# Performance work log

Measured on AMD Instinct MI355X. Metric: run time of the kernel, lower is better.

The kernel has to match this reference:

```python
import jax, jax.numpy as jnp
import numpy as np

FACTOR = 5


def setup_inputs() -> dict:
    key = jax.random.key(0)
    k1, k2, k3, k4 = jax.random.split(key, 4)
    B, L, H, D = 2, 4096, 8, 64
    sample_k = min(FACTOR * int(np.ceil(np.log(L))), L)  # 45
    return {
        "queries": jax.random.normal(k1, (B, L, H, D), dtype=jnp.float32),
        "keys": jax.random.normal(k2, (B, L, H, D), dtype=jnp.float32),
        "values": jax.random.normal(k3, (B, L, H, D), dtype=jnp.float32),
        "attn_mask": jnp.zeros((1,), dtype=bool),  # unused; ProbMask is built internally
        "index_sample": jax.random.randint(k4, (L, sample_k), 0, L, dtype=jnp.int32),
    }


def reference(queries, keys, values, attn_mask, index_sample):
    # queries/keys/values: [B, L, H, D] -> [B, H, L, D]
    Q = jnp.swapaxes(queries, 1, 2)
    K = jnp.swapaxes(keys, 1, 2)
    V = jnp.swapaxes(values, 1, 2)
    B, H, L_Q, D = Q.shape
    L_K = K.shape[2]
    n_top = min(FACTOR * int(np.ceil(np.log(L_Q))), L_Q)
    scale = 1.0 / jnp.sqrt(jnp.float32(D))

    # --- sparse measurement: sampled QK scores ---
    # K_sample[b,h,q,s,d] = K[b,h,index_sample[q,s],d]
    K_sample = K[:, :, index_sample, :]                       # [B,H,L_Q,S,D]
    QK_sample = jnp.einsum("bhqd,bhqsd->bhqs", Q, K_sample)   # [B,H,L_Q,S]
    M = QK_sample.max(axis=-1) - QK_sample.sum(axis=-1) / L_K  # sparsity measure

    # --- top-u query selection ---
    _, M_top = jax.lax.top_k(M, n_top)                         # [B,H,u]
    Q_reduce = jnp.take_along_axis(Q, M_top[..., None], axis=2)  # [B,H,u,D]

    # --- full scores for selected queries ---
    scores = jnp.einsum("bhud,bhkd->bhuk", Q_reduce, K) * scale  # [B,H,u,L_K]

    # mask_flag=True: causal ProbMask (key pos > selected query pos)
    key_pos = jnp.arange(L_K)
    causal = key_pos[None, None, None, :] > M_top[..., None]
    scores = jnp.where(causal, -jnp.inf, scores)
    attn = jax.nn.softmax(scores, axis=-1)

    # --- initial context (cumsum, masked case) + scatter update ---
    context = jnp.cumsum(V, axis=2)                            # [B,H,L_Q,D]
    ctx_sel = jnp.einsum("bhuk,bhkd->bhud", attn, V)
    b_idx = jnp.arange(B)[:, None, None]
    h_idx = jnp.arange(H)[None, :, None]
    context = context.at[b_idx, h_idx, M_top].set(ctx_sel)
    return jnp.swapaxes(context, 1, 2)  # [B, L_Q, H, D]
```

## Files before the change

kernel.cpp:

```cpp
#include <hip/hip_runtime.h>
#include <math.h>

#define B_    2
#define L_    4096
#define H_    8
#define D_    64
#define S_    45
#define NT_   45
#define BH_   16
#define CHV   64
#define NCHV  64
#define KC    128
#define NKC   32
#define SCALE 0.125f
#define NEG_BIG (-1e30f)

#define OFF_M     0
#define OFF_MTOP  65536
#define OFF_MPART 66304
#define OFF_SPART 89344
#define OFF_CTXP  112384
#define OFF_VSUM  112384

template <int CTRL>
__device__ __forceinline__ float dpp_ror_f(float x) {
    int y = __builtin_amdgcn_update_dpp(0, __float_as_int(x), CTRL, 0xF, 0xF, false);
    return __int_as_float(y);
}

__device__ __forceinline__ unsigned short f2bf(float x) {
    return (unsigned short)(__float_as_uint(x) >> 16);
}
__device__ __forceinline__ float bflo(unsigned u) { return __uint_as_float(u << 16); }
__device__ __forceinline__ float bfhi(unsigned u) { return __uint_as_float(u & 0xffff0000u); }

__global__ __launch_bounds__(256) void k1(const float* __restrict__ Q,
                                          const float* __restrict__ Kt,
                                          const float* __restrict__ V,
                                          const int* __restrict__ samp,
                                          float* __restrict__ ws)
{
    int tid  = threadIdx.x;
    int w    = tid >> 6;
    int lane = tid & 63;

    if (blockIdx.x < 4096) {
        int i   = blockIdx.x;
        int xcd = i & 7;
        int b   = xcd >> 2;
        int hh  = (xcd >> 1) & 1;
        int qq  = ((i >> 3) << 1) | (xcd & 1);

        __shared__ int soff[4][S_];
        if (tid < 4 * S_) {
            int qs = tid / S_, ss = tid - qs * S_;
            soff[qs][ss] = samp[(qq * 4 + qs) * S_ + ss] << 11;
        }
        __syncthreads();

        int q  = qq * 4 + w;
        int h4 = lane >> 4;

        const float4 q4 = *(const float4*)(Q +
            ((((long)b * L_ + q) * H_ + hh * 4) << 6) + lane * 4);

        const char* kb_base = (const char*)Kt +
            (long)b * L_ * 2048 + hh * 1024 + lane * 16;

        float mx = NEG_BIG, sm = 0.f;
#pragma unroll
        for (int jb = 0; jb < 45; jb += 15) {
            float4 kb[15];
#pragma unroll
            for (int j = 0; j < 15; ++j)
                kb[j] = *(const float4*)(kb_base + soff[w][jb + j]);
#pragma unroll
            for (int j = 0; j < 15; ++j) {
                float p = q4.x * kb[j].x + q4.y * kb[j].y +
                          q4.z * kb[j].z + q4.w * kb[j].w;
                p += dpp_ror_f<0x121>(p);
                p += dpp_ror_f<0x122>(p);
                p += dpp_ror_f<0x124>(p);
                p += dpp_ror_f<0x128>(p);
                mx = fmaxf(mx, p);
                sm += p;
            }
        }
        if ((lane & 15) == 0)
            ws[OFF_M + ((long)(b * 8 + hh * 4 + h4)) * L_ + q] =
                mx - sm * (1.0f / (float)L_);
    } else {
        int unit = (blockIdx.x - 4096) * 4 + w;
        int bh = unit >> 6, ch = unit & 63;
        int b = bh >> 3, h = bh & 7;
        const float* vp = V + ((((long)b * L_ + (long)ch * CHV) * H_ + h) << 6) + lane;
        float ssum = 0.f;
#pragma unroll
        for (int ib = 0; ib < CHV; ib += 16) {
            float vb[16];
#pragma unroll
            for (int j = 0; j < 16; ++j) vb[j] = vp[(long)(ib + j) * (H_ * D_)];
#pragma unroll
            for (int j = 0; j < 16; ++j) ssum += vb[j];
        }
        ws[OFF_VSUM + unit * 64 + lane] = ssum;
    }
}

__global__ __launch_bounds__(256) void k2(const float* __restrict__ V,
                                          float* __restrict__ out,
                                          float* __restrict__ ws)
{
    int tid  = threadIdx.x;
    int w    = tid >> 6;
    int lane = tid & 63;

    if (blockIdx.x < 16) {
        int bh = blockIdx.x;
        int* Mtop = (int*)ws + OFF_MTOP + bh * NT_;

        __shared__ float lv_[4][NT_];
        __shared__ int   li_[4][NT_];

        const float4* m4 = (const float4*)(ws + OFF_M + (long)bh * L_ +
                                           w * 1024 + lane * 16);
        float vals[16];
        {
            float4 a = m4[0], bq = m4[1], c = m4[2], d = m4[3];
            vals[0]=a.x; vals[1]=a.y; vals[2]=a.z; vals[3]=a.w;
            vals[4]=bq.x; vals[5]=bq.y; vals[6]=bq.z; vals[7]=bq.w;
            vals[8]=c.x; vals[9]=c.y; vals[10]=c.z; vals[11]=c.w;
            vals[12]=d.x; vals[13]=d.y; vals[14]=d.z; vals[15]=d.w;
        }
        float lv = NEG_BIG; int li = lane * 16;
#pragma unroll
        for (int j = 0; j < 16; ++j)
            if (vals[j] > lv) { lv = vals[j]; li = lane * 16 + j; }

        for (int r = 0; r < NT_; ++r) {
            float rm = lv;
            rm = fmaxf(rm, dpp_ror_f<0x121>(rm));
            rm = fmaxf(rm, dpp_ror_f<0x122>(rm));
            rm = fmaxf(rm, dpp_ror_f<0x124>(rm));
            rm = fmaxf(rm, dpp_ror_f<0x128>(rm));
            rm = fmaxf(rm, __shfl_xor(rm, 16));
            rm = fmaxf(rm, __shfl_xor(rm, 32));
            unsigned long long bm = __ballot(lv == rm);
            int winner = __ffsll(bm) - 1;
            int wi = __shfl(li, winner);
            if (lane == 0) { lv_[w][r] = rm; li_[w][r] = w * 1024 + wi; }
            if (lane == winner) {
#pragma unroll
                for (int j = 0; j < 16; ++j)
                    if (j == (wi & 15)) vals[j] = NEG_BIG;
                lv = NEG_BIG; li = lane * 16;
#pragma unroll
                for (int j = 0; j < 16; ++j)
                    if (vals[j] > lv) { lv = vals[j]; li = lane * 16 + j; }
            }
        }
        __syncthreads();

        if (w == 0) {
            int g = lane & 3;
            int p = 0;
            float hv = lv_[g][0]; int hi = li_[g][0];
            for (int r = 0; r < NT_; ++r) {
                float v0 = __shfl(hv, 0), v1 = __shfl(hv, 1),
                      v2 = __shfl(hv, 2), v3 = __shfl(hv, 3);
                int   i0 = __shfl(hi, 0), i1 = __shfl(hi, 1),
                      i2 = __shfl(hi, 2), i3 = __shfl(hi, 3);
                float bv = v0; int bi = i0, bg = 0;
                if (v1 > bv) { bv = v1; bi = i1; bg = 1; }
                if (v2 > bv) { bv = v2; bi = i2; bg = 2; }
                if (v3 > bv) { bv = v3; bi = i3; bg = 3; }
                if (lane == 0) Mtop[r] = bi;
                if (g == bg) {
                    ++p;
                    hv = (p < NT_) ? lv_[g][p] : NEG_BIG;
                    hi = (p < NT_) ? li_[g][p] : 0;
                }
            }
        }
    } else {
        int unit = (blockIdx.x - 16) * 4 + w;
        int bh = unit >> 6, ch = unit & 63;
        int b = bh >> 3, h = bh & 7;
        int d = lane;

        float acc = 0.f;
        {
            const float* vs = ws + OFF_VSUM + (long)bh * NCHV * 64 + d;
            int c = 0;
            for (; c + 8 <= ch; c += 8) {
                float vb[8];
#pragma unroll
                for (int j = 0; j < 8; ++j) vb[j] = vs[(c + j) * 64];
#pragma unroll
                for (int j = 0; j < 8; ++j) acc += vb[j];
            }
            for (; c < ch; ++c) acc += vs[c * 64];
        }

        const float* vp = V   + ((((long)b * L_ + (long)ch * CHV) * H_ + h) << 6) + d;
        float*       op = out + ((((long)b * L_ + (long)ch * CHV) * H_ + h) << 6) + d;
#pragma unroll
        for (int ib = 0; ib < CHV; ib += 16) {
            float vb[16];
#pragma unroll
            for (int j = 0; j < 16; ++j) vb[j] = vp[(long)(ib + j) * (H_ * D_)];
#pragma unroll
            for (int j = 0; j < 16; ++j) {
                acc += vb[j];
                op[(long)(ib + j) * (H_ * D_)] = acc;
            }
        }
    }
}

#define KPAD16 72
#define NUH    23
__global__ __launch_bounds__(256) void kC(const float* __restrict__ Q,
                                          const float* __restrict__ Kt,
                                          const float* __restrict__ V,
                                          float* __restrict__ ws)
{
    __shared__ unsigned short Klds16[KC * KPAD16];
    __shared__ unsigned short P16[NUH * KC];
    __shared__ int qpos[NUH];

    int tid = threadIdx.x;
    int bh = blockIdx.x >> 6;
    int kc = (blockIdx.x >> 1) & 31;
    int ug = blockIdx.x & 1;
    int b = bh >> 3, h = bh & 7;
    int kbase = kc * KC;
    int u0 = ug * 23;
    int NU = ug ? 22 : 23;

    if (tid < NU) qpos[tid] = ((const int*)ws)[OFF_MTOP + bh * NT_ + tid + u0];

    {
        const float4* ksrc4 = (const float4*)(Kt + ((((long)b * L_ + kbase) * H_ + h) << 6));
#pragma unroll
        for (int i = 0; i < 8; ++i) {
            int e = i * 256 + tid;
            int r = e >> 4, c4 = e & 15;
            float4 kv = ksrc4[(long)r * (H_ * D_ / 4) + c4];
            uint2 pk;
            pk.x = (__float_as_uint(kv.x) >> 16) | (__float_as_uint(kv.y) & 0xffff0000u);
            pk.y = (__float_as_uint(kv.z) >> 16) | (__float_as_uint(kv.w) & 0xffff0000u);
            *(uint2*)&Klds16[r * KPAD16 + c4 * 4] = pk;
        }
    }
    __syncthreads();

    int k = tid & 127, uh = tid >> 7;
    int kpos = kbase + k;
    {
        float kf[64];
#pragma unroll
        for (int j = 0; j < 8; ++j) {
            uint4 U = *(const uint4*)&Klds16[k * KPAD16 + j * 8];
            kf[j*8+0] = bflo(U.x); kf[j*8+1] = bfhi(U.x);
            kf[j*8+2] = bflo(U.y); kf[j*8+3] = bfhi(U.y);
            kf[j*8+4] = bflo(U.z); kf[j*8+5] = bfhi(U.z);
            kf[j*8+6] = bflo(U.w); kf[j*8+7] = bfhi(U.w);
        }

#pragma unroll 3
        for (int j = 0; j < 12; ++j) {
            int ul = uh * 12 + j;
            if (ul > NU - 1) ul = NU - 1;
            int qp_ = __builtin_amdgcn_readfirstlane(qpos[ul]);
            const float4* qrow = (const float4*)(Q + ((((long)b * L_ + qp_) * H_ + h) << 6));
            float a0 = 0.f, a1 = 0.f, a2 = 0.f, a3 = 0.f;
#pragma unroll
            for (int jj = 0; jj < 16; jj += 4) {
                float4 q0 = qrow[jj + 0], q1 = qrow[jj + 1];
                float4 q2 = qrow[jj + 2], q3 = qrow[jj + 3];
                a0 += q0.x * kf[jj*4+ 0] + q0.y * kf[jj*4+ 1] +
                      q0.z * kf[jj*4+ 2] + q0.w * kf[jj*4+ 3];
                a1 += q1.x * kf[jj*4+ 4] + q1.y * kf[jj*4+ 5] +
                      q1.z * kf[jj*4+ 6] + q1.w * kf[jj*4+ 7];
                a2 += q2.x * kf[jj*4+ 8] + q2.y * kf[jj*4+ 9] +
                      q2.z * kf[jj*4+10] + q2.w * kf[jj*4+11];
                a3 += q3.x * kf[jj*4+12] + q3.y * kf[jj*4+13] +
                      q3.z * kf[jj*4+14] + q3.w * kf[jj*4+15];
            }
            float sc = ((a0 + a1) + (a2 + a3)) * SCALE;
            if (kpos > qp_) sc = NEG_BIG;
            P16[ul * KC + k] = f2bf(sc);
        }
    }
    __syncthreads();

    int lane = tid & 63, w = tid >> 6;
    for (int ul = w; ul < NU; ul += 4) {
        float s0 = bflo(P16[ul * KC + lane]);
        float s1 = bflo(P16[ul * KC + 64 + lane]);
        float m = fmaxf(s0, s1);
#pragma unroll
        for (int off = 32; off; off >>= 1) m = fmaxf(m, __shfl_xor(m, off));
        float e0 = __expf(s0 - m), e1 = __expf(s1 - m);
        unsigned short b0 = f2bf(e0), b1 = f2bf(e1);
        P16[ul * KC + lane]      = b0;
        P16[ul * KC + 64 + lane] = b1;
        float sm = bflo(b0) + bflo(b1);
#pragma unroll
        for (int off = 32; off; off >>= 1) sm += __shfl_xor(sm, off);
        if (lane == 0) {
            ws[OFF_MPART + ((long)bh * NT_ + u0 + ul) * NKC + kc] = m;
            ws[OFF_SPART + ((long)bh * NT_ + u0 + ul) * NKC + kc] = sm;
        }
    }
    __syncthreads();

    {
        const float* vsrc = V + ((((long)b * L_ + kbase) * H_ + h) << 6);
        float ctx[6];
#pragma unroll
        for (int j = 0; j < 6; ++j) ctx[j] = 0.f;
        for (int kk8 = 0; kk8 < 16; ++kk8) {
            float v[8];
#pragma unroll
            for (int t = 0; t < 8; ++t)
                v[t] = vsrc[(long)(kk8 * 8 + t) * (H_ * D_) + lane];
#pragma unroll
            for (int j = 0; j < 6; ++j) {
                int ul = w + j * 4;
                if (ul < NU) {
                    uint4 U = *(const uint4*)&P16[ul * KC + kk8 * 8];
                    ctx[j] += bflo(U.x) * v[0] + bfhi(U.x) * v[1]
                            + bflo(U.y) * v[2] + bfhi(U.y) * v[3]
                            + bflo(U.z) * v[4] + bfhi(U.z) * v[5]
                            + bflo(U.w) * v[6] + bfhi(U.w) * v[7];
                }
            }
        }
#pragma unroll
        for (int j = 0; j < 6; ++j) {
            int ul = w + j * 4;
            if (ul < NU)
                ws[OFF_CTXP + ((long)(bh * NKC + kc) * NT_ + u0 + ul) * 64 + lane] = ctx[j];
        }
    }
}

__global__ __launch_bounds__(64) void kD(float* __restrict__ out,
                                         const float* __restrict__ ws)
{
    int lane = threadIdx.x;
    int unit = blockIdx.x;
    int bh = unit / NT_, u = unit - bh * NT_;
    int b = bh >> 3, h = bh & 7;

    const float4* mp4 = (const float4*)(ws + OFF_MPART + ((long)bh * NT_ + u) * NKC);
    const float4* sp4 = (const float4*)(ws + OFF_SPART + ((long)bh * NT_ + u) * NKC);

    float mc[NKC], sc[NKC];
    float m = NEG_BIG;
#pragma unroll
    for (int c4 = 0; c4 < NKC / 4; ++c4) {
        float4 mv = mp4[c4];
        float4 sv = sp4[c4];
        mc[c4 * 4 + 0] = mv.x; mc[c4 * 4 + 1] = mv.y;
        mc[c4 * 4 + 2] = mv.z; mc[c4 * 4 + 3] = mv.w;
        sc[c4 * 4 + 0] = sv.x; sc[c4 * 4 + 1] = sv.y;
        sc[c4 * 4 + 2] = sv.z; sc[c4 * 4 + 3] = sv.w;
        m = fmaxf(m, fmaxf(fmaxf(mv.x, mv.y), fmaxf(mv.z, mv.w)));
    }
    float T = 0.f, ctx = 0.f;
#pragma unroll
    for (int c = 0; c < NKC; ++c) {
        float wgt = __expf(mc[c] - m);
        T   += sc[c] * wgt;
        ctx += ws[OFF_CTXP + ((long)(bh * NKC + c) * NT_ + u) * 64 + lane] * wgt;
    }
    int qp = ((const int*)ws)[OFF_MTOP + bh * NT_ + u];
    out[((((long)b * L_ + qp) * H_ + h) << 6) + lane] = ctx / T;
}

extern "C" void kernel_launch(void* const* d_in, const int* in_sizes, int n_in,
                              void* d_out, int out_size, void* d_ws, size_t ws_size,
                              hipStream_t stream)
{
    const float* Q    = (const float*)d_in[0];
    const float* K    = (const float*)d_in[1];
    const float* V    = (const float*)d_in[2];
    const int*   samp = (const int*)d_in[4];
    float* out = (float*)d_out;
    float* ws  = (float*)d_ws;

    k1<<<4352, 256, 0, stream>>>(Q, K, V, samp, ws);
    k2<<<272, 256, 0, stream>>>(V, out, ws);
    kC<<<1024, 256, 0, stream>>>(Q, K, V, ws);
    kD<<<720, 64, 0, stream>>>(out, ws);
}
```

Baseline: 188.9 us.

## Process two queries per wave in sampling kernel and move cumsum into attention kernel

The sampled-score kernel now has each wave handle two queries, which halves its block count and gives each wave more independent gather loads in flight. The cumsum-output work moves out of the top-k kernel and into the attention kernel as extra blocks, so the top-k kernel runs only its 16 blocks and the cumsum overlaps with the attention blocks. The context-partial workspace offset is moved so it no longer aliases the V-sum region, which the cumsum blocks now read while attention blocks write partials. The cost is more register pressure per wave in the sampling kernel and extra shared-memory footprint reserved for the cumsum blocks in the attention kernel.

Result: slower. 196.5 us (+4.0%).

```diff
diff --git a/kernel.cpp b/kernel.cpp
--- a/kernel.cpp
+++ b/kernel.cpp
@@ -19,8 +19,8 @@
 #define OFF_MTOP  65536
 #define OFF_MPART 66304
 #define OFF_SPART 89344
-#define OFF_CTXP  112384
 #define OFF_VSUM  112384
+#define OFF_CTXP  177920
 
 template <int CTRL>
 __device__ __forceinline__ float dpp_ror_f(float x) {
@@ -44,53 +44,71 @@
     int w    = tid >> 6;
     int lane = tid & 63;
 
-    if (blockIdx.x < 4096) {
+    if (blockIdx.x < 2048) {
         int i   = blockIdx.x;
         int xcd = i & 7;
         int b   = xcd >> 2;
         int hh  = (xcd >> 1) & 1;
-        int qq  = ((i >> 3) << 1) | (xcd & 1);
-
-        __shared__ int soff[4][S_];
-        if (tid < 4 * S_) {
-            int qs = tid / S_, ss = tid - qs * S_;
-            soff[qs][ss] = samp[(qq * 4 + qs) * S_ + ss] << 11;
-        }
+        int qg  = ((i >> 3) << 1) | (xcd & 1);
+
+        __shared__ int soff[8 * S_];
+        for (int e = tid; e < 8 * S_; e += 256)
+            soff[e] = samp[qg * (8 * S_) + e] << 11;
         __syncthreads();
 
-        int q  = qq * 4 + w;
+        int qa = qg * 8 + w * 2;
         int h4 = lane >> 4;
 
-        const float4 q4 = *(const float4*)(Q +
-            ((((long)b * L_ + q) * H_ + hh * 4) << 6) + lane * 4);
+        const float4 qva = *(const float4*)(Q +
+            ((((long)b * L_ + qa)     * H_ + hh * 4) << 6) + lane * 4);
+        const float4 qvb = *(const float4*)(Q +
+            ((((long)b * L_ + qa + 1) * H_ + hh * 4) << 6) + lane * 4);
 
         const char* kb_base = (const char*)Kt +
             (long)b * L_ * 2048 + hh * 1024 + lane * 16;
-
-        float mx = NEG_BIG, sm = 0.f;
-#pragma unroll
-        for (int jb = 0; jb < 45; jb += 15) {
-            float4 kb[15];
-#pragma unroll
-            for (int j = 0; j < 15; ++j)
-                kb[j] = *(const float4*)(kb_base + soff[w][jb + j]);
-#pragma unroll
-            for (int j = 0; j < 15; ++j) {
-                float p = q4.x * kb[j].x + q4.y * kb[j].y +
-                          q4.z * kb[j].z + q4.w * kb[j].w;
+        const int* sa = &soff[(w * 2) * S_];
+        const int* sb = sa + S_;
+
+        float mxa = NEG_BIG, sma = 0.f, mxb = NEG_BIG, smb = 0.f;
+#pragma unroll
+        for (int jb = 0; jb < 45; jb += 9) {
+            float4 ka[9], kb[9];
+#pragma unroll
+            for (int j = 0; j < 9; ++j)
+                ka[j] = *(const float4*)(kb_base + sa[jb + j]);
+#pragma unroll
+            for (int j = 0; j < 9; ++j)
+                kb[j] = *(const float4*)(kb_base + sb[jb + j]);
+#pragma unroll
+            for (int j = 0; j < 9; ++j) {
+                float p = qva.x * ka[j].x + qva.y * ka[j].y +
+                          qva.z * ka[j].z + qva.w * ka[j].w;
                 p += dpp_ror_f<0x121>(p);
                 p += dpp_ror_f<0x122>(p);
                 p += dpp_ror_f<0x124>(p);
                 p += dpp_ror_f<0x128>(p);
-                mx = fmaxf(mx, p);
-                sm += p;
-            }
-        }
-        if ((lane & 15) == 0)
-            ws[OFF_M + ((long)(b * 8 + hh * 4 + h4)) * L_ + q] =
-                mx - sm * (1.0f / (float)L_);
+                mxa = fmaxf(mxa, p);
+                sma += p;
+            }
+#pragma unroll
+            for (int j = 0; j < 9; ++j) {
+                float p = qvb.x * kb[j].x + qvb.y * kb[j].y +
+                          qvb.z * kb[j].z + qvb.w * kb[j].w;
+                p += dpp_ror_f<0x121>(p);
+                p += dpp_ror_f<0x122>(p);
+                p += dpp_ror_f<0x124>(p);
+                p += dpp_ror_f<0x128>(p);
+                mxb = fmaxf(mxb, p);
+                smb += p;
+            }
+        }
+        if ((lane & 15) == 0) {
+            long base = (long)(b * 8 + hh * 4 + h4) * L_;
+            ws[OFF_M + base + qa]     = mxa - sma * (1.0f / (float)L_);
+            ws[OFF_M + base + qa + 1] = mxb - smb * (1.0f / (float)L_);
+        }
     } else {
-        int unit = (blockIdx.x - 4096) * 4 + w;
+        int unit = (blockIdx.x - 2048) * 4 + w;
         int bh = unit >> 6, ch = unit & 63;
         int b = bh >> 3, h = bh & 7;
         const float* vp = V + ((((long)b * L_ + (long)ch * CHV) * H_ + h) << 6) + lane;
@@ -107,86 +125,99 @@
     }
 }
 
-__global__ __launch_bounds__(256) void k2(const float* __restrict__ V,
-                                          float* __restrict__ out,
-                                          float* __restrict__ ws)
+__global__ __launch_bounds__(256) void k2(float* __restrict__ ws)
 {
     int tid  = threadIdx.x;
     int w    = tid >> 6;
     int lane = tid & 63;
 
-    if (blockIdx.x < 16) {
-        int bh = blockIdx.x;
-        int* Mtop = (int*)ws + OFF_MTOP + bh * NT_;
-
-        __shared__ float lv_[4][NT_];
-        __shared__ int   li_[4][NT_];
-
-        const float4* m4 = (const float4*)(ws + OFF_M + (long)bh * L_ +
-                                           w * 1024 + lane * 16);
-        float vals[16];
-        {
-            float4 a = m4[0], bq = m4[1], c = m4[2], d = m4[3];
-            vals[0]=a.x; vals[1]=a.y; vals[2]=a.z; vals[3]=a.w;
-            vals[4]=bq.x; vals[5]=bq.y; vals[6]=bq.z; vals[7]=bq.w;
-            vals[8]=c.x; vals[9]=c.y; vals[10]=c.z; vals[11]=c.w;
-            vals[12]=d.x; vals[13]=d.y; vals[14]=d.z; vals[15]=d.w;
-        }
-        float lv = NEG_BIG; int li = lane * 16;
-#pragma unroll
-        for (int j = 0; j < 16; ++j)
-            if (vals[j] > lv) { lv = vals[j]; li = lane * 16 + j; }
-
+    int bh = blockIdx.x;
+    int* Mtop = (int*)ws + OFF_MTOP + bh * NT_;
+
+    __shared__ float lv_[4][NT_];
+    __shared__ int   li_[4][NT_];
+
+    const float4* m4 = (const float4*)(ws + OFF_M + (long)bh * L_ +
+                                       w * 1024 + lane * 16);
+    float vals[16];
+    {
+        float4 a = m4[0], bq = m4[1], c = m4[2], d = m4[3];
+        vals[0]=a.x; vals[1]=a.y; vals[2]=a.z; vals[3]=a.w;
+        vals[4]=bq.x; vals[5]=bq.y; vals[6]=bq.z; vals[7]=bq.w;
+        vals[8]=c.x; vals[9]=c.y; vals[10]=c.z; vals[11]=c.w;
+        vals[12]=d.x; vals[13]=d.y; vals[14]=d.z; vals[15]=d.w;
+    }
+    float lv = NEG_BIG; int li = lane * 16;
+#pragma unroll
+    for (int j = 0; j < 16; ++j)
+        if (vals[j] > lv) { lv = vals[j]; li = lane * 16 + j; }
+
+    for (int r = 0; r < NT_; ++r) {
+        float rm = lv;
+        rm = fmaxf(rm, dpp_ror_f<0x121>(rm));
+        rm = fmaxf(rm, dpp_ror_f<0x122>(rm));
+        rm = fmaxf(rm, dpp_ror_f<0x124>(rm));
+        rm = fmaxf(rm, dpp_ror_f<0x128>(rm));
+        rm = fmaxf(rm, __shfl_xor(rm, 16));
+        rm = fmaxf(rm, __shfl_xor(rm, 32));
+        unsigned long long bm = __ballot(lv == rm);
+        int winner = __ffsll(bm) - 1;
+        int wi = __shfl(li, winner);
+        if (lane == 0) { lv_[w][r] = rm; li_[w][r] = w * 1024 + wi; }
+        if (lane == winner) {
+#pragma unroll
+            for (int j = 0; j < 16; ++j)
+                if (j == (wi & 15)) vals[j] = NEG_BIG;
+            lv = NEG_BIG; li = lane * 16;
+#pragma unroll
+            for (int j = 0; j < 16; ++j)
+                if (vals[j] > lv) { lv = vals[j]; li = lane * 16 + j; }
+        }
+    }
+    __syncthreads();
+
+    if (w == 0) {
+        int g = lane & 3;
+        int p = 0;
+        float hv = lv_[g][0]; int hi = li_[g][0];
         for (int r = 0; r < NT_; ++r) {
-            float rm = lv;
-            rm = fmaxf(rm, dpp_ror_f<0x121>(rm));
-            rm = fmaxf(rm, dpp_ror_f<0x122>(rm));
-            rm = fmaxf(rm, dpp_ror_f<0x124>(rm));
-            rm = fmaxf(rm, dpp_ror_f<0x128>(rm));
-            rm = fmaxf(rm, __shfl_xor(rm, 16));
-            rm = fmaxf(rm, __shfl_xor(rm, 32));
-            unsigned long long bm = __ballot(lv == rm);
-            int winner = __ffsll(bm) - 1;
-            int wi = __shfl(li, winner);
-            if (lane == 0) { lv_[w][r] = rm; li_[w][r] = w * 1024 + wi; }
-            if (lane == winner) {
-#pragma unroll
-                for (int j = 0; j < 16; ++j)
-                    if (j == (wi & 15)) vals[j] = NEG_BIG;
-                lv = NEG_BIG; li = lane * 16;
-#pragma unroll
-                for (int j = 0; j < 16; ++j)
-                    if (vals[j] > lv) { lv = vals[j]; li = lane * 16 + j; }
-            }
-        }
-        __syncthreads();
-
-        if (w == 0) {
-            int g = lane & 3;
-            int p = 0;
-            float hv = lv_[g][0]; int hi = li_[g][0];
-            for (int r = 0; r < NT_; ++r) {
-                float v0 = __shfl(hv, 0), v1 = __shfl(hv, 1),
-                      v2 = __shfl(hv, 2), v3 = __shfl(hv, 3);
-                int   i0 = __shfl(hi, 0), i1 = __shfl(hi, 1),
-                      i2 = __shfl(hi, 2), i3 = __shfl(hi, 3);
-                float bv = v0; int bi = i0, bg = 0;
-                if (v1 > bv) { bv = v1; bi = i1; bg = 1; }
-                if (v2 > bv) { bv = v2; bi = i2; bg = 2; }
-                if (v3 > bv) { bv = v3; bi = i3; bg = 3; }
-                if (lane == 0) Mtop[r] = bi;
-                if (g == bg) {
-                    ++p;
-                    hv = (p < NT_) ? lv_[g][p] : NEG_BIG;
-                    hi = (p < NT_) ? li_[g][p] : 0;
-                }
-            }
-        }
-    } else {
-        int unit = (blockIdx.x - 16) * 4 + w;
+            float v0 = __shfl(hv, 0), v1 = __shfl(hv, 1),
+                  v2 = __shfl(hv, 2), v3 = __shfl(hv, 3);
+            int   i0 = __shfl(hi, 0), i1 = __shfl(hi, 1),
+                  i2 = __shfl(hi, 2), i3 = __shfl(hi, 3);
+            float bv = v0; int bi = i0, bg = 0;
+            if (v1 > bv) { bv = v1; bi = i1; bg = 1; }
+            if (v2 > bv) { bv = v2; bi = i2; bg = 2; }
+            if (v3 > bv) { bv = v3; bi = i3; bg = 3; }
+            if (lane == 0) Mtop[r] = bi;
+            if (g == bg) {
+                ++p;
+                hv = (p < NT_) ? lv_[g][p] : NEG_BIG;
+                hi = (p < NT_) ? li_[g][p] : 0;
+            }
+        }
+    }
+}
+
+#define KPAD16 72
+#define NUH    23
+__global__ __launch_bounds__(256) void k3(const float* __restrict__ Q,
+                                          const float* __restrict__ Kt,
+                                          const float* __restrict__ V,
+                                          float* __restrict__ out,
+                                          float* __restrict__ ws)
+{
+    __shared__ unsigned short Klds16[KC * KPAD16];
+    __shared__ unsigned short P16[NUH * KC];
+    __shared__ int qpos[NUH];
+
+    int tid = threadIdx.x;
+
+    if (blockIdx.x >= 1024) {
+        int w = tid >> 6, d = tid & 63;
+        int unit = (blockIdx.x - 1024) * 4 + w;
         int bh = unit >> 6, ch = unit & 63;
         int b = bh >> 3, h = bh & 7;
-        int d = lane;
 
         float acc = 0.f;
         {
@@ -215,21 +246,9 @@
                 op[(long)(ib + j) * (H_ * D_)] = acc;
             }
         }
-    }
-}
-
-#define KPAD16 72
-#define NUH    23
-__global__ __launch_bounds__(256) void kC(const float* __restrict__ Q,
-                                          const float* __restrict__ Kt,
-                                          const float* __restrict__ V,
-                                          float* __restrict__ ws)
-{
-    __shared__ unsigned short Klds16[KC * KPAD16];
-    __shared__ unsigned short P16[NUH * KC];
-    __shared__ int qpos[NUH];
-
-    int tid = threadIdx.x;
+        return;
+    }
+
     int bh = blockIdx.x >> 6;
     int kc = (blockIdx.x >> 1) & 31;
     int ug = blockIdx.x & 1;
@@ -392,8 +411,8 @@
     float* out = (float*)d_out;
     float* ws  = (float*)d_ws;
 
-    k1<<<4352, 256, 0, stream>>>(Q, K, V, samp, ws);
-    k2<<<272, 256, 0, stream>>>(V, out, ws);
-    kC<<<1024, 256, 0, stream>>>(Q, K, V, ws);
+    k1<<<2304, 256, 0, stream>>>(Q, K, V, samp, ws);
+    k2<<<16, 256, 0, stream>>>(ws);
+    k3<<<1280, 256, 0, stream>>>(Q, K, V, out, ws);
     kD<<<720, 64, 0, stream>>>(out, ws);
 }
```

## Skip fully causal-masked key chunks and overlap cumsum with attention kernel

Applied to the files above, without the earlier changes.

The prefix-sum output pass moves out of the top-k kernel and into extra blocks of the attention kernel. The top-k kernel now launches only its 16 selection blocks, and the cumsum writes can overlap the score and PV work. Inside the attention kernel, any selected query whose position lies before the key chunk skips its QK dot products and writes masked scores directly. Waves with no active queries skip the PV accumulation and the partial-context stores. The context-partials workspace gets its own offset so it no longer aliases the V chunk sums that are now read concurrently. The combining kernel still reads partial contexts for skipped chunks, which are left unwritten, so it relies on their zero weights to cancel them.

New measurement: 189.4 us. About the same (+0.3%).

```diff
diff --git a/kernel.cpp b/kernel.cpp
--- a/kernel.cpp
+++ b/kernel.cpp
@@ -19,8 +19,8 @@
 #define OFF_MTOP  65536
 #define OFF_MPART 66304
 #define OFF_SPART 89344
-#define OFF_CTXP  112384
 #define OFF_VSUM  112384
+#define OFF_CTXP  177920
 
 template <int CTRL>
 __device__ __forceinline__ float dpp_ror_f(float x) {
@@ -107,86 +107,99 @@
     }
 }
 
-__global__ __launch_bounds__(256) void k2(const float* __restrict__ V,
-                                          float* __restrict__ out,
-                                          float* __restrict__ ws)
+__global__ __launch_bounds__(256) void k2(float* __restrict__ ws)
 {
     int tid  = threadIdx.x;
     int w    = tid >> 6;
     int lane = tid & 63;
 
-    if (blockIdx.x < 16) {
-        int bh = blockIdx.x;
-        int* Mtop = (int*)ws + OFF_MTOP + bh * NT_;
-
-        __shared__ float lv_[4][NT_];
-        __shared__ int   li_[4][NT_];
-
-        const float4* m4 = (const float4*)(ws + OFF_M + (long)bh * L_ +
-                                           w * 1024 + lane * 16);
-        float vals[16];
-        {
-            float4 a = m4[0], bq = m4[1], c = m4[2], d = m4[3];
-            vals[0]=a.x; vals[1]=a.y; vals[2]=a.z; vals[3]=a.w;
-            vals[4]=bq.x; vals[5]=bq.y; vals[6]=bq.z; vals[7]=bq.w;
-            vals[8]=c.x; vals[9]=c.y; vals[10]=c.z; vals[11]=c.w;
-            vals[12]=d.x; vals[13]=d.y; vals[14]=d.z; vals[15]=d.w;
-        }
-        float lv = NEG_BIG; int li = lane * 16;
-#pragma unroll
-        for (int j = 0; j < 16; ++j)
-            if (vals[j] > lv) { lv = vals[j]; li = lane * 16 + j; }
-
+    int bh = blockIdx.x;
+    int* Mtop = (int*)ws + OFF_MTOP + bh * NT_;
+
+    __shared__ float lv_[4][NT_];
+    __shared__ int   li_[4][NT_];
+
+    const float4* m4 = (const float4*)(ws + OFF_M + (long)bh * L_ +
+                                       w * 1024 + lane * 16);
+    float vals[16];
+    {
+        float4 a = m4[0], bq = m4[1], c = m4[2], d = m4[3];
+        vals[0]=a.x; vals[1]=a.y; vals[2]=a.z; vals[3]=a.w;
+        vals[4]=bq.x; vals[5]=bq.y; vals[6]=bq.z; vals[7]=bq.w;
+        vals[8]=c.x; vals[9]=c.y; vals[10]=c.z; vals[11]=c.w;
+        vals[12]=d.x; vals[13]=d.y; vals[14]=d.z; vals[15]=d.w;
+    }
+    float lv = NEG_BIG; int li = lane * 16;
+#pragma unroll
+    for (int j = 0; j < 16; ++j)
+        if (vals[j] > lv) { lv = vals[j]; li = lane * 16 + j; }
+
+    for (int r = 0; r < NT_; ++r) {
+        float rm = lv;
+        rm = fmaxf(rm, dpp_ror_f<0x121>(rm));
+        rm = fmaxf(rm, dpp_ror_f<0x122>(rm));
+        rm = fmaxf(rm, dpp_ror_f<0x124>(rm));
+        rm = fmaxf(rm, dpp_ror_f<0x128>(rm));
+        rm = fmaxf(rm, __shfl_xor(rm, 16));
+        rm = fmaxf(rm, __shfl_xor(rm, 32));
+        unsigned long long bm = __ballot(lv == rm);
+        int winner = __ffsll(bm) - 1;
+        int wi = __shfl(li, winner);
+        if (lane == 0) { lv_[w][r] = rm; li_[w][r] = w * 1024 + wi; }
+        if (lane == winner) {
+#pragma unroll
+            for (int j = 0; j < 16; ++j)
+                if (j == (wi & 15)) vals[j] = NEG_BIG;
+            lv = NEG_BIG; li = lane * 16;
+#pragma unroll
+            for (int j = 0; j < 16; ++j)
+                if (vals[j] > lv) { lv = vals[j]; li = lane * 16 + j; }
+        }
+    }
+    __syncthreads();
+
+    if (w == 0) {
+        int g = lane & 3;
+        int p = 0;
+        float hv = lv_[g][0]; int hi = li_[g][0];
         for (int r = 0; r < NT_; ++r) {
-            float rm = lv;
-            rm = fmaxf(rm, dpp_ror_f<0x121>(rm));
-            rm = fmaxf(rm, dpp_ror_f<0x122>(rm));
-            rm = fmaxf(rm, dpp_ror_f<0x124>(rm));
-            rm = fmaxf(rm, dpp_ror_f<0x128>(rm));
-            rm = fmaxf(rm, __shfl_xor(rm, 16));
-            rm = fmaxf(rm, __shfl_xor(rm, 32));
-            unsigned long long bm = __ballot(lv == rm);
-            int winner = __ffsll(bm) - 1;
-            int wi = __shfl(li, winner);
-            if (lane == 0) { lv_[w][r] = rm; li_[w][r] = w * 1024 + wi; }
-            if (lane == winner) {
-#pragma unroll
-                for (int j = 0; j < 16; ++j)
-                    if (j == (wi & 15)) vals[j] = NEG_BIG;
-                lv = NEG_BIG; li = lane * 16;
-#pragma unroll
-                for (int j = 0; j < 16; ++j)
-                    if (vals[j] > lv) { lv = vals[j]; li = lane * 16 + j; }
-            }
-        }
-        __syncthreads();
-
-        if (w == 0) {
-            int g = lane & 3;
-            int p = 0;
-            float hv = lv_[g][0]; int hi = li_[g][0];
-            for (int r = 0; r < NT_; ++r) {
-                float v0 = __shfl(hv, 0), v1 = __shfl(hv, 1),
-                      v2 = __shfl(hv, 2), v3 = __shfl(hv, 3);
-                int   i0 = __shfl(hi, 0), i1 = __shfl(hi, 1),
-                      i2 = __shfl(hi, 2), i3 = __shfl(hi, 3);
-                float bv = v0; int bi = i0, bg = 0;
-                if (v1 > bv) { bv = v1; bi = i1; bg = 1; }
-                if (v2 > bv) { bv = v2; bi = i2; bg = 2; }
-                if (v3 > bv) { bv = v3; bi = i3; bg = 3; }
-                if (lane == 0) Mtop[r] = bi;
-                if (g == bg) {
-                    ++p;
-                    hv = (p < NT_) ? lv_[g][p] : NEG_BIG;
-                    hi = (p < NT_) ? li_[g][p] : 0;
-                }
-            }
-        }
-    } else {
-        int unit = (blockIdx.x - 16) * 4 + w;
+            float v0 = __shfl(hv, 0), v1 = __shfl(hv, 1),
+                  v2 = __shfl(hv, 2), v3 = __shfl(hv, 3);
+            int   i0 = __shfl(hi, 0), i1 = __shfl(hi, 1),
+                  i2 = __shfl(hi, 2), i3 = __shfl(hi, 3);
+            float bv = v0; int bi = i0, bg = 0;
+            if (v1 > bv) { bv = v1; bi = i1; bg = 1; }
+            if (v2 > bv) { bv = v2; bi = i2; bg = 2; }
+            if (v3 > bv) { bv = v3; bi = i3; bg = 3; }
+            if (lane == 0) Mtop[r] = bi;
+            if (g == bg) {
+                ++p;
+                hv = (p < NT_) ? lv_[g][p] : NEG_BIG;
+                hi = (p < NT_) ? li_[g][p] : 0;
+            }
+        }
+    }
+}
+
+#define KPAD16 72
+#define NUH    23
+__global__ __launch_bounds__(256) void k3(const float* __restrict__ Q,
+                                          const float* __restrict__ Kt,
+                                          const float* __restrict__ V,
+                                          float* __restrict__ out,
+                                          float* __restrict__ ws)
+{
+    __shared__ unsigned short Klds16[KC * KPAD16];
+    __shared__ unsigned short P16[NUH * KC];
+    __shared__ int qpos[NUH];
+
+    int tid = threadIdx.x;
+
+    if (blockIdx.x >= 1024) {
+        int w = tid >> 6, d = tid & 63;
+        int unit = (blockIdx.x - 1024) * 4 + w;
         int bh = unit >> 6, ch = unit & 63;
         int b = bh >> 3, h = bh & 7;
-        int d = lane;
 
         float acc = 0.f;
         {
@@ -215,21 +228,9 @@
                 op[(long)(ib + j) * (H_ * D_)] = acc;
             }
         }
-    }
-}
-
-#define KPAD16 72
-#define NUH    23
-__global__ __launch_bounds__(256) void kC(const float* __restrict__ Q,
-                                          const float* __restrict__ Kt,
-                                          const float* __restrict__ V,
-                                          float* __restrict__ ws)
-{
-    __shared__ unsigned short Klds16[KC * KPAD16];
-    __shared__ unsigned short P16[NUH * KC];
-    __shared__ int qpos[NUH];
-
-    int tid = threadIdx.x;
+        return;
+    }
+
     int bh = blockIdx.x >> 6;
     int kc = (blockIdx.x >> 1) & 31;
     int ug = blockIdx.x & 1;
@@ -273,6 +274,10 @@
             int ul = uh * 12 + j;
             if (ul > NU - 1) ul = NU - 1;
             int qp_ = __builtin_amdgcn_readfirstlane(qpos[ul]);
+            if (kbase > qp_) {
+                P16[ul * KC + k] = f2bf(NEG_BIG);
+                continue;
+            }
             const float4* qrow = (const float4*)(Q + ((((long)b * L_ + qp_) * H_ + h) << 6));
             float a0 = 0.f, a1 = 0.f, a2 = 0.f, a3 = 0.f;
 #pragma unroll
@@ -318,31 +323,41 @@
 
     {
         const float* vsrc = V + ((((long)b * L_ + kbase) * H_ + h) << 6);
-        float ctx[6];
-#pragma unroll
-        for (int j = 0; j < 6; ++j) ctx[j] = 0.f;
-        for (int kk8 = 0; kk8 < 16; ++kk8) {
-            float v[8];
-#pragma unroll
-            for (int t = 0; t < 8; ++t)
-                v[t] = vsrc[(long)(kk8 * 8 + t) * (H_ * D_) + lane];
+        bool act[6];
+        int nact = 0;
+#pragma unroll
+        for (int j = 0; j < 6; ++j) {
+            int ul = w + j * 4;
+            act[j] = (ul < NU) && (kbase <= qpos[ul]);
+            nact += act[j] ? 1 : 0;
+        }
+        if (nact) {
+            float ctx[6];
+#pragma unroll
+            for (int j = 0; j < 6; ++j) ctx[j] = 0.f;
+            for (int kk8 = 0; kk8 < 16; ++kk8) {
+                float v[8];
+#pragma unroll
+                for (int t = 0; t < 8; ++t)
+                    v[t] = vsrc[(long)(kk8 * 8 + t) * (H_ * D_) + lane];
+#pragma unroll
+                for (int j = 0; j < 6; ++j) {
+                    if (act[j]) {
+                        int ul = w + j * 4;
+                        uint4 U = *(const uint4*)&P16[ul * KC + kk8 * 8];
+                        ctx[j] += bflo(U.x) * v[0] + bfhi(U.x) * v[1]
+                                + bflo(U.y) * v[2] + bfhi(U.y) * v[3]
+                                + bflo(U.z) * v[4] + bfhi(U.z) * v[5]
+                                + bflo(U.w) * v[6] + bfhi(U.w) * v[7];
+                    }
+                }
+            }
 #pragma unroll
             for (int j = 0; j < 6; ++j) {
                 int ul = w + j * 4;
-                if (ul < NU) {
-                    uint4 U = *(const uint4*)&P16[ul * KC + kk8 * 8];
-                    ctx[j] += bflo(U.x) * v[0] + bfhi(U.x) * v[1]
-                            + bflo(U.y) * v[2] + bfhi(U.y) * v[3]
-                            + bflo(U.z) * v[4] + bfhi(U.z) * v[5]
-                            + bflo(U.w) * v[6] + bfhi(U.w) * v[7];
-                }
-            }
-        }
-#pragma unroll
-        for (int j = 0; j < 6; ++j) {
-            int ul = w + j * 4;
-            if (ul < NU)
-                ws[OFF_CTXP + ((long)(bh * NKC + kc) * NT_ + u0 + ul) * 64 + lane] = ctx[j];
+                if (act[j])
+                    ws[OFF_CTXP + ((long)(bh * NKC + kc) * NT_ + u0 + ul) * 64 + lane] = ctx[j];
+            }
         }
     }
 }
@@ -393,7 +408,7 @@
     float* ws  = (float*)d_ws;
 
     k1<<<4352, 256, 0, stream>>>(Q, K, V, samp, ws);
-    k2<<<272, 256, 0, stream>>>(V, out, ws);
-    kC<<<1024, 256, 0, stream>>>(Q, K, V, ws);
+    k2<<<16, 256, 0, stream>>>(ws);
+    k3<<<1280, 256, 0, stream>>>(Q, K, V, out, ws);
     kD<<<720, 64, 0, stream>>>(out, ws);
 }
```
